# Performance work log

Measured on AMD Instinct MI355X. Metric: run time of the kernel, lower is better.

## Reference

```python
import jax, jax.numpy as jnp
import numpy as np

B, T, V, E, H, L = 32, 128, 32000, 256, 256, 2


def setup_inputs() -> dict:
    key = jax.random.key(0)
    ks = jax.random.split(key, 9)
    s = 0.05  # weight scale to keep gates out of deep saturation
    x = jax.random.randint(ks[0], (B, T), 0, V, dtype=jnp.int32)
    return {
        "x": x,
        "embed_table": jax.random.normal(ks[1], (V, E), jnp.float32) * 0.1,
        "fW": jax.random.normal(ks[2], (L, E, 4 * H), jnp.float32) * s,
        "fU": jax.random.normal(ks[3], (L, H, 4 * H), jnp.float32) * s,
        "fb": jnp.zeros((L, 4 * H), jnp.float32),
        "bW": jax.random.normal(ks[4], (L, E, 4 * H), jnp.float32) * s,
        "bU": jax.random.normal(ks[5], (L, H, 4 * H), jnp.float32) * s,
        "bb": jnp.zeros((L, 4 * H), jnp.float32),
        "Wp": jax.random.normal(ks[6], (2 * H, V), jnp.float32) * s,
        "bp": jnp.zeros((V,), jnp.float32),
        "Wn": jax.random.normal(ks[7], ((T - 2) * 2 * H, 2), jnp.float32) * s,
        "bn": jnp.zeros((2,), jnp.float32),
    }


def run_stacked_lstm(emb, mask, W, U, b):
    """emb: [B,S,D], mask: [B,S] bool. Keras LSTMCell gate order (i,f,g,o);
    masked steps carry state through (output = previous top-layer h)."""
    nL = W.shape[0]
    Bz = emb.shape[0]
    Hd = U.shape[1]
    emb_t = jnp.swapaxes(emb, 0, 1)   # [S,B,D]
    mask_t = jnp.swapaxes(mask, 0, 1)  # [S,B]
    h0 = jnp.zeros((nL, Bz, Hd), emb.dtype)

    def step(carry, inp):
        hs, cs = carry
        x_t, m_t = inp
        m = m_t[:, None]
        new_h, new_c = [], []
        inp_x = x_t
        for l in range(nL):
            z = inp_x @ W[l] + hs[l] @ U[l] + b[l]
            i, f, g, o = jnp.split(z, 4, axis=-1)
            c = jax.nn.sigmoid(f) * cs[l] + jax.nn.sigmoid(i) * jnp.tanh(g)
            h = jax.nn.sigmoid(o) * jnp.tanh(c)
            h = jnp.where(m, h, hs[l])
            c = jnp.where(m, c, cs[l])
            new_h.append(h)
            new_c.append(c)
            inp_x = h
        return (jnp.stack(new_h), jnp.stack(new_c)), inp_x

    _, ys = jax.lax.scan(step, (h0, h0), (emb_t, mask_t))
    return jnp.swapaxes(ys, 0, 1)  # [B,S,H]


def reference(x, embed_table, fW, fU, fb, bW, bU, bb, Wp, bp, Wn, bn):
    o = embed_table[x]            # [B,T,E]
    mask = x != 0                 # mask_zero=True
    # forward LSTM over tokens 0..T-2
    f = run_stacked_lstm(o[:, :-1], mask[:, :-1], fW, fU, fb)
    # backward LSTM (go_backwards=True): run over reversed o[:,1:];
    # Keras RNN leaves outputs in reversed-time order.
    b_out = run_stacked_lstm(o[:, 1:][:, ::-1], mask[:, 1:][:, ::-1], bW, bU, bb)
    ctx = jnp.concatenate([f[:, :-1], b_out[:, 1:]], axis=-1)  # [B,T-2,2H]
    word_logits = ctx @ Wp + bp                                 # [B,T-2,V]
    nsp_logits = ctx.reshape(ctx.shape[0], -1) @ Wn + bn        # [B,2]
    return word_logits, nsp_logits
```

## Files before the change

kernel.cpp:

```cpp
#include <hip/hip_runtime.h>
#include <stdint.h>

typedef __bf16 bf16;
typedef __bf16 bf16x8 __attribute__((ext_vector_type(8)));
typedef float  f32x4  __attribute__((ext_vector_type(4)));

#define NB 16
#define OFF_MF     0
#define OFF_MB     4096
#define OFF_H0F    8192
#define TAG_ONE    (128*32*256*4)
#define OFF_H0B    (OFF_H0F + 1*TAG_ONE)
#define OFF_H1F    (OFF_H0F + 2*TAG_ONE)
#define OFF_H1B    (OFF_H0F + 3*TAG_ONE)
#define OFF_XF     (OFF_H0F + 4*TAG_ONE)
#define XF_BYTES   (4064*256*2)
#define OFF_XB     (OFF_XF + XF_BYTES)
#define OFF_FW0T   (OFF_XB + XF_BYTES)
#define W0T_BYTES  (1024*256*2)
#define OFF_BW0T   (OFF_FW0T + W0T_BYTES)
#define OFF_PRE0F  (OFF_BW0T + W0T_BYTES)
#define PRE_BYTES  (4064*1024*4)
#define OFF_PRE0B  (OFF_PRE0F + PRE_BYTES)
#define OFF_WPT    OFF_PRE0F
#define OFF_CTX    OFF_XF

__device__ __forceinline__ int swz8(int row, int kblk) { return (kblk ^ (row & 7)) << 3; }

__device__ __forceinline__ uint64_t sys_load_u64(const uint64_t* p) {
  return __hip_atomic_load(p, __ATOMIC_RELAXED, __HIP_MEMORY_SCOPE_SYSTEM);
}
__device__ __forceinline__ void sys_store_u32(uint32_t* p, uint32_t v) {
  __hip_atomic_store(p, v, __ATOMIC_RELAXED, __HIP_MEMORY_SCOPE_SYSTEM);
}

typedef __attribute__((address_space(1))) unsigned int as1_u32;
typedef __attribute__((address_space(3))) unsigned int as3_u32;
__device__ __forceinline__ void gload16(const void* g, void* l) {
  __builtin_amdgcn_global_load_lds((as1_u32*)g, (as3_u32*)l, 16, 0, 0);
}

__global__ __launch_bounds__(256) void embed_kernel(
    const int* __restrict__ x, const float* __restrict__ tab,
    bf16* __restrict__ xf, bf16* __restrict__ xb,
    unsigned char* __restrict__ mf, unsigned char* __restrict__ mb)
{
  int t = blockIdx.x;
  int b = blockIdx.y;
  int k = threadIdx.x;
  int tokf = x[b*128 + t];
  int tokb = x[b*128 + 127 - t];
  xf[(size_t)(t*32+b)*256 + k] = (bf16)tab[(size_t)tokf*256 + k];
  xb[(size_t)(t*32+b)*256 + k] = (bf16)tab[(size_t)tokb*256 + k];
  if (k == 0) { mf[t*32+b] = (tokf != 0); mb[t*32+b] = (tokb != 0); }
}

__global__ __launch_bounds__(256) void transpose_to_bf16(
    const float* __restrict__ in, bf16* __restrict__ out, int R, int C)
{
  __shared__ float tile[64][65];
  int c0 = blockIdx.x*64, r0 = blockIdx.y*64;
  int tid = threadIdx.x;
  int r = tid >> 2, cs = (tid & 3)*16;
  #pragma unroll
  for (int i = 0; i < 16; i += 4) {
    float4 v = *(const float4*)(in + (size_t)(r0+r)*C + c0 + cs + i);
    tile[r][cs+i+0]=v.x; tile[r][cs+i+1]=v.y; tile[r][cs+i+2]=v.z; tile[r][cs+i+3]=v.w;
  }
  __syncthreads();
  int c = tid >> 2, rs = (tid & 3)*16;
  #pragma unroll
  for (int i = 0; i < 16; ++i)
    out[(size_t)(c0+c)*R + r0 + rs + i] = (bf16)tile[rs+i][c];
}

__global__ __launch_bounds__(256) void gemm_bf16(
    const bf16* __restrict__ A, const bf16* __restrict__ BT,
    const float* __restrict__ bias, float* __restrict__ C,
    int M, int N, int K)
{
  __shared__ bf16 As[128][64];
  __shared__ bf16 Bs[128][64];
  int tid = threadIdx.x;
  int row0 = blockIdx.x*128, col0 = blockIdx.y*128;
  int wave = tid >> 6, lane = tid & 63, l15 = lane & 15, quad = lane >> 4;
  int wm = (wave & 1)*64, wn = (wave >> 1)*64;
  int lr = lane >> 3;
  int lc = (lane & 7)*8;
  f32x4 acc[4][4] = {};
  for (int kk = 0; kk < K; kk += 64) {
    #pragma unroll
    for (int i = 0; i < 4; ++i) {
      int rb = (wave*4 + i)*8;
      int ga = row0 + rb + lr; if (ga > M-1) ga = M-1;
      gload16(A  + (size_t)ga*K + kk + lc,                 &As[rb][0]);
      gload16(BT + (size_t)(col0 + rb + lr)*K + kk + lc,   &Bs[rb][0]);
    }
    __syncthreads();
    #pragma unroll
    for (int ks = 0; ks < 64; ks += 32) {
      bf16x8 af[4], bfr[4];
      #pragma unroll
      for (int mi = 0; mi < 4; ++mi) af[mi]  = *(const bf16x8*)&As[wm + mi*16 + l15][ks + quad*8];
      #pragma unroll
      for (int ni = 0; ni < 4; ++ni) bfr[ni] = *(const bf16x8*)&Bs[wn + ni*16 + l15][ks + quad*8];
      #pragma unroll
      for (int mi = 0; mi < 4; ++mi)
        #pragma unroll
        for (int ni = 0; ni < 4; ++ni)
          acc[mi][ni] = __builtin_amdgcn_mfma_f32_16x16x32_bf16(af[mi], bfr[ni], acc[mi][ni], 0, 0, 0);
    }
    __syncthreads();
  }
  #pragma unroll
  for (int ni = 0; ni < 4; ++ni) {
    int col = col0 + wn + ni*16 + l15;
    float bv = bias[col];
    #pragma unroll
    for (int mi = 0; mi < 4; ++mi) {
      int rbase = row0 + wm + mi*16 + quad*4;
      #pragma unroll
      for (int r = 0; r < 4; ++r) {
        int grow = rbase + r;
        if (grow < M) C[(size_t)grow*N + col] = acc[mi][ni][r] + bv;
      }
    }
  }
}

__global__ __launch_bounds__(512) void recur_kernel(
    const float* __restrict__ pre0f, const float* __restrict__ pre0b,
    const float* __restrict__ fU0, const float* __restrict__ bU0,
    const float* __restrict__ fW1, const float* __restrict__ fU1,
    const float* __restrict__ bW1, const float* __restrict__ bU1,
    const float* __restrict__ fb1, const float* __restrict__ bb1,
    const unsigned char* __restrict__ mf, const unsigned char* __restrict__ mb,
    uint32_t* __restrict__ h0f, uint32_t* __restrict__ h0b,
    uint32_t* __restrict__ h1f, uint32_t* __restrict__ h1b)
{
  __shared__ bf16 U_T[64][512];
  __shared__ bf16 hA[32][512];
  __shared__ float z_s[32][65];

  int tid = threadIdx.x;
  int bx = blockIdx.x;
  int dir = bx >> 5, stage = (bx >> 4) & 1, blk = bx & 15;
  int j0 = blk * 16;
  const float* pre = dir ? pre0b : pre0f;
  const unsigned char* mgl = dir ? mb : mf;
  uint32_t* h0 = dir ? h0b : h0f;
  uint32_t* h1 = dir ? h1b : h1f;
  uint32_t* hout = stage ? h1 : h0;

  if (stage == 0) {
    const float* U = dir ? bU0 : fU0;
    for (int idx = tid; idx < 64*256; idx += 512) {
      int k = idx >> 6, c = idx & 63;
      int gc = (c >> 4)*256 + j0 + (c & 15);
      U_T[c][swz8(c, k >> 3) | (k & 7)] = (bf16)U[(size_t)k*1024 + gc];
    }
  } else {
    const float* W = dir ? bW1 : fW1;
    const float* U = dir ? bU1 : fU1;
    for (int idx = tid; idx < 64*512; idx += 512) {
      int k = idx >> 6, c = idx & 63;
      int gc = (c >> 4)*256 + j0 + (c & 15);
      float v = (k < 256) ? W[(size_t)k*1024 + gc] : U[(size_t)(k-256)*1024 + gc];
      U_T[c][swz8(c, k >> 3) | (k & 7)] = (bf16)v;
    }
  }

  int gb = tid >> 4, gu = tid & 15;
  float c_state = 0.f, h_state = 0.f;
  float bi = 0.f, bff = 0.f, bgg = 0.f, boo = 0.f;
  if (stage == 1) {
    const float* bias = dir ? bb1 : fb1;
    bi  = bias[0*256 + j0 + gu];
    bff = bias[1*256 + j0 + gu];
    bgg = bias[2*256 + j0 + gu];
    boo = bias[3*256 + j0 + gu];
  }
  int wave = tid >> 6, lane = tid & 63, l15 = lane & 15, quad = lane >> 4;
  int m0 = (wave & 1)*16, n0 = (wave >> 1)*16;

  int laddr[16];
  #pragma unroll
  for (int j = 0; j < 16; ++j) {
    int g = (j & 7)*512 + tid;
    int kb = g >> 8, rem = g & 255;
    int row = rem >> 3, up = (rem & 7)*2;
    int p = (j >> 3)*256 + kb*16 + up;
    laddr[j] = row*512 + swz8(row, p >> 3) + (p & 7);
  }
  bf16* hAf = &hA[0][0];
  __syncthreads();

  for (int t = 0; t < 127; ++t) {
    float p_i = bi, p_f = bff, p_g = bgg, p_o = boo;
    if (stage == 0) {
      const float* p = pre + ((size_t)t*32 + gb)*1024 + j0 + gu;
      p_i = p[0]; p_f = p[256]; p_g = p[512]; p_o = p[768];
    }
    unsigned char msk = mgl[t*32 + gb];

    uint64_t v[16];
    if (stage == 0) {
      const uint64_t* s0 = (const uint64_t*)h0 + (size_t)t*4096;
      if (t > 0) {
        #pragma unroll
        for (int j = 0; j < 8; ++j) v[j] = sys_load_u64(s0 + (j*512 + tid));
        uint64_t pat = ((uint64_t)t << 48) | ((uint64_t)t << 16);
        #pragma unroll
        for (int j = 0; j < 8; ++j) {
          int sp = 0;
          while ((v[j] & 0xFFFF0000FFFF0000ull) != pat) {
            if (++sp > 1024) __builtin_amdgcn_s_sleep(2);
            if (sp > (1<<22)) break;
            v[j] = sys_load_u64(s0 + (j*512 + tid));
          }
        }
      } else {
        #pragma unroll
        for (int j = 0; j < 8; ++j) v[j] = 0;
      }
      #pragma unroll
      for (int j = 0; j < 8; ++j) {
        uint32_t pk = (uint32_t)(v[j] & 0xFFFF) | ((uint32_t)((v[j] >> 32) & 0xFFFF) << 16);
        *(uint32_t*)&hAf[laddr[j]] = pk;
      }
    } else {
      const uint64_t* s0 = (const uint64_t*)h0 + (size_t)(t+1)*4096;
      const uint64_t* s1 = (const uint64_t*)h1 + (size_t)t*4096;
      #pragma unroll
      for (int j = 0; j < 8; ++j) v[j] = sys_load_u64(s0 + (j*512 + tid));
      if (t > 0) {
        #pragma unroll
        for (int j = 8; j < 16; ++j) v[j] = sys_load_u64(s1 + ((j-8)*512 + tid));
      } else {
        #pragma unroll
        for (int j = 8; j < 16; ++j) v[j] = 0;
      }
      uint64_t pat0 = ((uint64_t)(t+1) << 48) | ((uint64_t)(t+1) << 16);
      #pragma unroll
      for (int j = 0; j < 8; ++j) {
        int sp = 0;
        while ((v[j] & 0xFFFF0000FFFF0000ull) != pat0) {
          if (++sp > 1024) __builtin_amdgcn_s_sleep(2);
          if (sp > (1<<22)) break;
          v[j] = sys_load_u64(s0 + (j*512 + tid));
        }
      }
      if (t > 0) {
        uint64_t pat1 = ((uint64_t)t << 48) | ((uint64_t)t << 16);
        #pragma unroll
        for (int j = 8; j < 16; ++j) {
          int sp = 0;
          while ((v[j] & 0xFFFF0000FFFF0000ull) != pat1) {
            if (++sp > 1024) __builtin_amdgcn_s_sleep(2);
            if (sp > (1<<22)) break;
            v[j] = sys_load_u64(s1 + ((j-8)*512 + tid));
          }
        }
      }
      #pragma unroll
      for (int j = 0; j < 16; ++j) {
        uint32_t pk = (uint32_t)(v[j] & 0xFFFF) | ((uint32_t)((v[j] >> 32) & 0xFFFF) << 16);
        *(uint32_t*)&hAf[laddr[j]] = pk;
      }
    }
    __syncthreads();

    f32x4 zac;
    {
      f32x4 a0 = {0.f,0.f,0.f,0.f}, a1 = {0.f,0.f,0.f,0.f};
      if (stage == 0) {
        #pragma unroll
        for (int kc = 0; kc < 128; kc += 32) {
          int kb = (kc >> 3) + quad;
          a0 = __builtin_amdgcn_mfma_f32_16x16x32_bf16(
                 *(const bf16x8*)&hA[m0 + l15][swz8(m0 + l15, kb)],
                 *(const bf16x8*)&U_T[n0 + l15][swz8(n0 + l15, kb)], a0, 0, 0, 0);
        }
        #pragma unroll
        for (int kc = 128; kc < 256; kc += 32) {
          int kb = (kc >> 3) + quad;
          a1 = __builtin_amdgcn_mfma_f32_16x16x32_bf16(
                 *(const bf16x8*)&hA[m0 + l15][swz8(m0 + l15, kb)],
                 *(const bf16x8*)&U_T[n0 + l15][swz8(n0 + l15, kb)], a1, 0, 0, 0);
        }
      } else {
        #pragma unroll
        for (int kc = 0; kc < 256; kc += 32) {
          int kb = (kc >> 3) + quad;
          a0 = __builtin_amdgcn_mfma_f32_16x16x32_bf16(
                 *(const bf16x8*)&hA[m0 + l15][swz8(m0 + l15, kb)],
                 *(const bf16x8*)&U_T[n0 + l15][swz8(n0 + l15, kb)], a0, 0, 0, 0);
        }
        #pragma unroll
        for (int kc = 256; kc < 512; kc += 32) {
          int kb = (kc >> 3) + quad;
          a1 = __builtin_amdgcn_mfma_f32_16x16x32_bf16(
                 *(const bf16x8*)&hA[m0 + l15][swz8(m0 + l15, kb)],
                 *(const bf16x8*)&U_T[n0 + l15][swz8(n0 + l15, kb)], a1, 0, 0, 0);
        }
      }
      zac = a0 + a1;
    }
    #pragma unroll
    for (int r = 0; r < 4; ++r) z_s[m0 + quad*4 + r][n0 + l15] = zac[r];
    __syncthreads();

    float zi = z_s[gb][ 0 + gu] + p_i;
    float zf = z_s[gb][16 + gu] + p_f;
    float zg = z_s[gb][32 + gu] + p_g;
    float zo = z_s[gb][48 + gu] + p_o;
    float ig = 1.f/(1.f + expf(-zi));
    float fg = 1.f/(1.f + expf(-zf));
    float gg = tanhf(zg);
    float og = 1.f/(1.f + expf(-zo));
    float cn = fg*c_state + ig*gg;
    float hn = og*tanhf(cn);
    if (msk) { c_state = cn; h_state = hn; }

    bf16 hv = (bf16)h_state;
    unsigned short hb;
    __builtin_memcpy(&hb, &hv, 2);
    uint32_t val = ((uint32_t)(t+1) << 16) | (uint32_t)hb;
    sys_store_u32(hout + (size_t)(t+1)*8192 + blk*512 + tid, val);
  }
}

__global__ __launch_bounds__(256) void ctx_kernel(
    const uint32_t* __restrict__ h1f, const uint32_t* __restrict__ h1b, bf16* __restrict__ ctx)
{
  int tau = blockIdx.x;
  int b = blockIdx.y;
  int k = threadIdx.x;
  size_t r = (size_t)(b*126 + tau)*512;
  uint32_t vf = h1f[(size_t)(tau+1)*8192 + (k>>4)*512 + b*16 + (k&15)];
  uint32_t vb = h1b[(size_t)(tau+2)*8192 + (k>>4)*512 + b*16 + (k&15)];
  ((unsigned short*)ctx)[r + k]       = (unsigned short)(vf & 0xFFFF);
  ((unsigned short*)ctx)[r + 256 + k] = (unsigned short)(vb & 0xFFFF);
}

__global__ __launch_bounds__(256) void nsp_kernel(
    const bf16* __restrict__ ctx, const float* __restrict__ Wn,
    const float* __restrict__ bn, float* __restrict__ out)
{
  int b = blockIdx.x, tid = threadIdx.x;
  const unsigned short* cb = (const unsigned short*)ctx;
  float a0 = 0.f, a1 = 0.f;
  for (int flat = tid; flat < 64512; flat += 256) {
    int tau = flat >> 9, k = flat & 511;
    float cv = __uint_as_float((unsigned)cb[(size_t)(b*126 + tau)*512 + k] << 16);
    float2 w = *(const float2*)(Wn + 2*(size_t)flat);
    a0 += cv*w.x; a1 += cv*w.y;
  }
  __shared__ float r0[256], r1[256];
  r0[tid] = a0; r1[tid] = a1;
  __syncthreads();
  for (int s = 128; s > 0; s >>= 1) {
    if (tid < s) { r0[tid] += r0[tid+s]; r1[tid] += r1[tid+s]; }
    __syncthreads();
  }
  if (tid == 0) { out[b*2+0] = r0[0] + bn[0]; out[b*2+1] = r1[0] + bn[1]; }
}

extern "C" void kernel_launch(void* const* d_in, const int* in_sizes, int n_in,
                              void* d_out, int out_size, void* d_ws, size_t ws_size,
                              hipStream_t stream)
{
  const int*   x   = (const int*)d_in[0];
  const float* tab = (const float*)d_in[1];
  const float* fW  = (const float*)d_in[2];
  const float* fU  = (const float*)d_in[3];
  const float* fb  = (const float*)d_in[4];
  const float* bW  = (const float*)d_in[5];
  const float* bU  = (const float*)d_in[6];
  const float* bb  = (const float*)d_in[7];
  const float* Wp  = (const float*)d_in[8];
  const float* bp  = (const float*)d_in[9];
  const float* Wn  = (const float*)d_in[10];
  const float* bn  = (const float*)d_in[11];
  float* out = (float*)d_out;
  char* ws = (char*)d_ws;

  unsigned char* mf = (unsigned char*)(ws + OFF_MF);
  unsigned char* mb = (unsigned char*)(ws + OFF_MB);
  uint32_t* h0f = (uint32_t*)(ws + OFF_H0F);
  uint32_t* h0b = (uint32_t*)(ws + OFF_H0B);
  uint32_t* h1f = (uint32_t*)(ws + OFF_H1F);
  uint32_t* h1b = (uint32_t*)(ws + OFF_H1B);
  bf16* xf    = (bf16*)(ws + OFF_XF);
  bf16* xb    = (bf16*)(ws + OFF_XB);
  bf16* fW0T  = (bf16*)(ws + OFF_FW0T);
  bf16* bW0T  = (bf16*)(ws + OFF_BW0T);
  float* pre0f = (float*)(ws + OFF_PRE0F);
  float* pre0b = (float*)(ws + OFF_PRE0B);
  bf16* WpT   = (bf16*)(ws + OFF_WPT);
  bf16* ctx   = (bf16*)(ws + OFF_CTX);

  hipMemsetAsync(ws + OFF_H0F, 0, 4*(size_t)TAG_ONE, stream);

  embed_kernel<<<dim3(127, 32), 256, 0, stream>>>(x, tab, xf, xb, mf, mb);

  transpose_to_bf16<<<dim3(16, 4),  256, 0, stream>>>(fW, fW0T, 256, 1024);
  transpose_to_bf16<<<dim3(16, 4),  256, 0, stream>>>(bW, bW0T, 256, 1024);

  gemm_bf16<<<dim3(32, 8), 256, 0, stream>>>(xf, fW0T, fb, pre0f, 4064, 1024, 256);
  gemm_bf16<<<dim3(32, 8), 256, 0, stream>>>(xb, bW0T, bb, pre0b, 4064, 1024, 256);

  recur_kernel<<<64, 512, 0, stream>>>(
      pre0f, pre0b,
      fU, bU,
      fW + 262144, fU + 262144, bW + 262144, bU + 262144,
      fb + 1024, bb + 1024,
      mf, mb, h0f, h0b, h1f, h1b);

  transpose_to_bf16<<<dim3(500, 8), 256, 0, stream>>>(Wp, WpT, 512, 32000);

  ctx_kernel<<<dim3(126, 32), 256, 0, stream>>>(h1f, h1b, ctx);

  gemm_bf16<<<dim3(32, 250), 256, 0, stream>>>(ctx, WpT, bp, out, 4032, 32000, 512);

  nsp_kernel<<<32, 256, 0, stream>>>(ctx, Wn, bn, out + (size_t)4032*32000);
}
```

Baseline: 1.487 ms.

## Keep recurrent weights in registers and feed MFMA directly from polled global loads

The recurrent weight slice moves from shared memory into per-thread bf16x8 register fragments. Each wave now polls and loads its own A-operand chunks of h straight from global memory in MFMA layout, overlapping the spin-wait for later chunks with MFMAs on earlier ones. This removes the shared-memory staging of h and one barrier per step, and double-buffers z_s so only one barrier remains. In exchange it adds heavy register pressure (16 bf16x8 fragments plus 32 u64 load buffers), which may spill or reduce occupancy, and each wave issues redundant global loads.

```diff
diff --git a/kernel.cpp b/kernel.cpp
--- a/kernel.cpp
+++ b/kernel.cpp
@@ -25,8 +25,6 @@
 #define OFF_WPT    OFF_PRE0F
 #define OFF_CTX    OFF_XF
 
-__device__ __forceinline__ int swz8(int row, int kblk) { return (kblk ^ (row & 7)) << 3; }
-
 __device__ __forceinline__ uint64_t sys_load_u64(const uint64_t* p) {
   return __hip_atomic_load(p, __ATOMIC_RELAXED, __HIP_MEMORY_SCOPE_SYSTEM);
 }
@@ -38,6 +36,47 @@
 typedef __attribute__((address_space(3))) unsigned int as3_u32;
 __device__ __forceinline__ void gload16(const void* g, void* l) {
   __builtin_amdgcn_global_load_lds((as1_u32*)g, (as3_u32*)l, 16, 0, 0);
+}
+
+__device__ __forceinline__ void chunk_load(uint64_t g[4][4], const uint64_t* sb, int s0,
+                                           int quad, int brow) {
+  #pragma unroll
+  for (int s = 0; s < 4; ++s)
+    #pragma unroll
+    for (int d = 0; d < 4; ++d) {
+      int o = 4*(s0 + s) + quad;
+      g[s][d] = sys_load_u64(sb + ((o >> 1)*256 + brow*8 + (o & 1)*4 + d));
+    }
+}
+__device__ __forceinline__ bool chunk_ok(const uint64_t g[4][4], uint64_t want) {
+  uint64_t x = 0;
+  #pragma unroll
+  for (int s = 0; s < 4; ++s)
+    #pragma unroll
+    for (int d = 0; d < 4; ++d) x |= (g[s][d] ^ want) & 0xFFFF0000FFFF0000ull;
+  return x == 0;
+}
+__device__ __forceinline__ void chunk_wait(uint64_t g[4][4], const uint64_t* sb, int s0,
+                                           int quad, int brow, uint64_t want) {
+  int guard = 0;
+  while (!chunk_ok(g, want)) {
+    if (++guard > (1 << 18)) break;
+    if (guard > 64) __builtin_amdgcn_s_sleep(1);
+    chunk_load(g, sb, s0, quad, brow);
+  }
+}
+__device__ __forceinline__ void chunk_mfma(const uint64_t g[4][4], const bf16x8* Bf,
+                                           int sbase, f32x4& acc) {
+  #pragma unroll
+  for (int s = 0; s < 4; ++s) {
+    union { uint32_t u[4]; bf16x8 v; } A;
+    #pragma unroll
+    for (int d = 0; d < 4; ++d) {
+      uint64_t w = g[s][d];
+      A.u[d] = (uint32_t)(w & 0xFFFFu) | ((uint32_t)((w >> 32) & 0xFFFFu) << 16);
+    }
+    acc = __builtin_amdgcn_mfma_f32_16x16x32_bf16(A.v, Bf[sbase + s], acc, 0, 0, 0);
+  }
 }
 
 __global__ __launch_bounds__(256) void embed_kernel(
@@ -138,9 +177,7 @@
     uint32_t* __restrict__ h0f, uint32_t* __restrict__ h0b,
     uint32_t* __restrict__ h1f, uint32_t* __restrict__ h1b)
 {
-  __shared__ bf16 U_T[64][512];
-  __shared__ bf16 hA[32][512];
-  __shared__ float z_s[32][65];
+  __shared__ float z_s[2][32][65];
 
   int tid = threadIdx.x;
   int bx = blockIdx.x;
@@ -152,21 +189,34 @@
   uint32_t* h1 = dir ? h1b : h1f;
   uint32_t* hout = stage ? h1 : h0;
 
+  int wave = tid >> 6, lane = tid & 63, l15 = lane & 15, quad = lane >> 4;
+  int m0 = (wave & 1)*16, n0 = (wave >> 1)*16;
+  int brow = m0 + l15;
+  int gc = (wave >> 1)*256 + j0 + l15;
+
+  bf16x8 Bf[16];
   if (stage == 0) {
     const float* U = dir ? bU0 : fU0;
-    for (int idx = tid; idx < 64*256; idx += 512) {
-      int k = idx >> 6, c = idx & 63;
-      int gc = (c >> 4)*256 + j0 + (c & 15);
-      U_T[c][swz8(c, k >> 3) | (k & 7)] = (bf16)U[(size_t)k*1024 + gc];
+    #pragma unroll
+    for (int s = 0; s < 8; ++s) {
+      bf16x8 f;
+      #pragma unroll
+      for (int e = 0; e < 8; ++e) f[e] = (bf16)U[(size_t)((4*s+quad)*8 + e)*1024 + gc];
+      Bf[s] = f;
     }
   } else {
     const float* W = dir ? bW1 : fW1;
     const float* U = dir ? bU1 : fU1;
-    for (int idx = tid; idx < 64*512; idx += 512) {
-      int k = idx >> 6, c = idx & 63;
-      int gc = (c >> 4)*256 + j0 + (c & 15);
-      float v = (k < 256) ? W[(size_t)k*1024 + gc] : U[(size_t)(k-256)*1024 + gc];
-      U_T[c][swz8(c, k >> 3) | (k & 7)] = (bf16)v;
+    #pragma unroll
+    for (int s = 0; s < 16; ++s) {
+      bf16x8 f;
+      #pragma unroll
+      for (int e = 0; e < 8; ++e) {
+        int k = (4*s+quad)*8 + e;
+        float v = (k < 256) ? W[(size_t)k*1024 + gc] : U[(size_t)(k-256)*1024 + gc];
+        f[e] = (bf16)v;
+      }
+      Bf[s] = f;
     }
   }
 
@@ -180,21 +230,8 @@
     bgg = bias[2*256 + j0 + gu];
     boo = bias[3*256 + j0 + gu];
   }
-  int wave = tid >> 6, lane = tid & 63, l15 = lane & 15, quad = lane >> 4;
-  int m0 = (wave & 1)*16, n0 = (wave >> 1)*16;
-
-  int laddr[16];
-  #pragma unroll
-  for (int j = 0; j < 16; ++j) {
-    int g = (j & 7)*512 + tid;
-    int kb = g >> 8, rem = g & 255;
-    int row = rem >> 3, up = (rem & 7)*2;
-    int p = (j >> 3)*256 + kb*16 + up;
-    laddr[j] = row*512 + swz8(row, p >> 3) + (p & 7);
-  }
-  bf16* hAf = &hA[0][0];
-  __syncthreads();
-
+
+  int par = 0;
   for (int t = 0; t < 127; ++t) {
     float p_i = bi, p_f = bff, p_g = bgg, p_o = boo;
     if (stage == 0) {
@@ -203,117 +240,50 @@
     }
     unsigned char msk = mgl[t*32 + gb];
 
-    uint64_t v[16];
+    f32x4 a0 = {0.f,0.f,0.f,0.f}, a1 = {0.f,0.f,0.f,0.f};
+    uint64_t ga[4][4], gbuf[4][4];
+
     if (stage == 0) {
-      const uint64_t* s0 = (const uint64_t*)h0 + (size_t)t*4096;
       if (t > 0) {
-        #pragma unroll
-        for (int j = 0; j < 8; ++j) v[j] = sys_load_u64(s0 + (j*512 + tid));
-        uint64_t pat = ((uint64_t)t << 48) | ((uint64_t)t << 16);
-        #pragma unroll
-        for (int j = 0; j < 8; ++j) {
-          int sp = 0;
-          while ((v[j] & 0xFFFF0000FFFF0000ull) != pat) {
-            if (++sp > 1024) __builtin_amdgcn_s_sleep(2);
-            if (sp > (1<<22)) break;
-            v[j] = sys_load_u64(s0 + (j*512 + tid));
-          }
-        }
-      } else {
-        #pragma unroll
-        for (int j = 0; j < 8; ++j) v[j] = 0;
-      }
-      #pragma unroll
-      for (int j = 0; j < 8; ++j) {
-        uint32_t pk = (uint32_t)(v[j] & 0xFFFF) | ((uint32_t)((v[j] >> 32) & 0xFFFF) << 16);
-        *(uint32_t*)&hAf[laddr[j]] = pk;
+        const uint64_t* sp = (const uint64_t*)h0 + (size_t)t*4096;
+        uint64_t want = ((uint64_t)t << 48) | ((uint64_t)t << 16);
+        chunk_load(ga,   sp, 0, quad, brow);
+        chunk_load(gbuf, sp, 4, quad, brow);
+        chunk_wait(ga,   sp, 0, quad, brow, want);
+        chunk_mfma(ga,   Bf, 0, a0);
+        chunk_wait(gbuf, sp, 4, quad, brow, want);
+        chunk_mfma(gbuf, Bf, 4, a1);
       }
     } else {
-      const uint64_t* s0 = (const uint64_t*)h0 + (size_t)(t+1)*4096;
-      const uint64_t* s1 = (const uint64_t*)h1 + (size_t)t*4096;
-      #pragma unroll
-      for (int j = 0; j < 8; ++j) v[j] = sys_load_u64(s0 + (j*512 + tid));
+      const uint64_t* s0p = (const uint64_t*)h0 + (size_t)(t+1)*4096;
+      const uint64_t* s1p = (const uint64_t*)h1 + (size_t)t*4096;
+      uint64_t w0 = ((uint64_t)(t+1) << 48) | ((uint64_t)(t+1) << 16);
+      uint64_t w1 = ((uint64_t)t << 48) | ((uint64_t)t << 16);
+      chunk_load(ga,   s0p, 0, quad, brow);
+      chunk_load(gbuf, s0p, 4, quad, brow);
+      chunk_wait(ga,   s0p, 0, quad, brow, w0);
+      chunk_mfma(ga,   Bf, 0, a0);
+      if (t > 0) chunk_load(ga, s1p, 0, quad, brow);
+      chunk_wait(gbuf, s0p, 4, quad, brow, w0);
+      chunk_mfma(gbuf, Bf, 4, a0);
       if (t > 0) {
-        #pragma unroll
-        for (int j = 8; j < 16; ++j) v[j] = sys_load_u64(s1 + ((j-8)*512 + tid));
-      } else {
-        #pragma unroll
-        for (int j = 8; j < 16; ++j) v[j] = 0;
+        chunk_load(gbuf, s1p, 4, quad, brow);
+        chunk_wait(ga,   s1p, 0, quad, brow, w1);
+        chunk_mfma(ga,   Bf, 8, a1);
+        chunk_wait(gbuf, s1p, 4, quad, brow, w1);
+        chunk_mfma(gbuf, Bf, 12, a1);
       }
-      uint64_t pat0 = ((uint64_t)(t+1) << 48) | ((uint64_t)(t+1) << 16);
-      #pragma unroll
-      for (int j = 0; j < 8; ++j) {
-        int sp = 0;
-        while ((v[j] & 0xFFFF0000FFFF0000ull) != pat0) {
-          if (++sp > 1024) __builtin_amdgcn_s_sleep(2);
-          if (sp > (1<<22)) break;
-          v[j] = sys_load_u64(s0 + (j*512 + tid));
-        }
-      }
-      if (t > 0) {
-        uint64_t pat1 = ((uint64_t)t << 48) | ((uint64_t)t << 16);
-        #pragma unroll
-        for (int j = 8; j < 16; ++j) {
-          int sp = 0;
-          while ((v[j] & 0xFFFF0000FFFF0000ull) != pat1) {
-            if (++sp > 1024) __builtin_amdgcn_s_sleep(2);
-            if (sp > (1<<22)) break;
-            v[j] = sys_load_u64(s1 + ((j-8)*512 + tid));
-          }
-        }
-      }
-      #pragma unroll
-      for (int j = 0; j < 16; ++j) {
-        uint32_t pk = (uint32_t)(v[j] & 0xFFFF) | ((uint32_t)((v[j] >> 32) & 0xFFFF) << 16);
-        *(uint32_t*)&hAf[laddr[j]] = pk;
-      }
-    }
+    }
+
+    f32x4 zac = a0 + a1;
+    #pragma unroll
+    for (int r = 0; r < 4; ++r) z_s[par][m0 + quad*4 + r][n0 + l15] = zac[r];
     __syncthreads();
 
-    f32x4 zac;
-    {
-      f32x4 a0 = {0.f,0.f,0.f,0.f}, a1 = {0.f,0.f,0.f,0.f};
-      if (stage == 0) {
-        #pragma unroll
-        for (int kc = 0; kc < 128; kc += 32) {
-          int kb = (kc >> 3) + quad;
-          a0 = __builtin_amdgcn_mfma_f32_16x16x32_bf16(
-                 *(const bf16x8*)&hA[m0 + l15][swz8(m0 + l15, kb)],
-                 *(const bf16x8*)&U_T[n0 + l15][swz8(n0 + l15, kb)], a0, 0, 0, 0);
-        }
-        #pragma unroll
-        for (int kc = 128; kc < 256; kc += 32) {
-          int kb = (kc >> 3) + quad;
-          a1 = __builtin_amdgcn_mfma_f32_16x16x32_bf16(
-                 *(const bf16x8*)&hA[m0 + l15][swz8(m0 + l15, kb)],
-                 *(const bf16x8*)&U_T[n0 + l15][swz8(n0 + l15, kb)], a1, 0, 0, 0);
-        }
-      } else {
-        #pragma unroll
-        for (int kc = 0; kc < 256; kc += 32) {
-          int kb = (kc >> 3) + quad;
-          a0 = __builtin_amdgcn_mfma_f32_16x16x32_bf16(
-                 *(const bf16x8*)&hA[m0 + l15][swz8(m0 + l15, kb)],
-                 *(const bf16x8*)&U_T[n0 + l15][swz8(n0 + l15, kb)], a0, 0, 0, 0);
-        }
-        #pragma unroll
-        for (int kc = 256; kc < 512; kc += 32) {
-          int kb = (kc >> 3) + quad;
-          a1 = __builtin_amdgcn_mfma_f32_16x16x32_bf16(
-                 *(const bf16x8*)&hA[m0 + l15][swz8(m0 + l15, kb)],
-                 *(const bf16x8*)&U_T[n0 + l15][swz8(n0 + l15, kb)], a1, 0, 0, 0);
-        }
-      }
-      zac = a0 + a1;
-    }
-    #pragma unroll
-    for (int r = 0; r < 4; ++r) z_s[m0 + quad*4 + r][n0 + l15] = zac[r];
-    __syncthreads();
-
-    float zi = z_s[gb][ 0 + gu] + p_i;
-    float zf = z_s[gb][16 + gu] + p_f;
-    float zg = z_s[gb][32 + gu] + p_g;
-    float zo = z_s[gb][48 + gu] + p_o;
+    float zi = z_s[par][gb][ 0 + gu] + p_i;
+    float zf = z_s[par][gb][16 + gu] + p_f;
+    float zg = z_s[par][gb][32 + gu] + p_g;
+    float zo = z_s[par][gb][48 + gu] + p_o;
     float ig = 1.f/(1.f + expf(-zi));
     float fg = 1.f/(1.f + expf(-zf));
     float gg = tanhf(zg);
@@ -327,6 +297,7 @@
     __builtin_memcpy(&hb, &hv, 2);
     uint32_t val = ((uint32_t)(t+1) << 16) | (uint32_t)hb;
     sys_store_u32(hout + (size_t)(t+1)*8192 + blk*512 + tid, val);
+    par ^= 1;
   }
 }
 
```

Result: slower. 2.257 ms (+51.8%).
